# Performance work log

Measured on AMD Instinct MI355X. Metric: run time of the kernel, lower is better.

The kernel has to match this reference:

```python
import jax, jax.numpy as jnp
import numpy as np

U = 4        # num_users
B = 64       # batch
N = 2048     # n_antennas (RIS elements)
F = 4        # feature_dim per user
H = 16       # local_info_dim + global_info_dim
LD = 8       # local_info_dim
GD = 8       # global_info_dim
CIN = F + 2 * H  # 36, input channels for layers 2-7 and final conv


def setup_inputs() -> dict:
    key = jax.random.key(0)
    ks = jax.random.split(key, 12)
    w = lambda k, s: (jax.random.normal(k, s, dtype=jnp.float32) * 0.1)
    return {
        "channel": jax.random.normal(ks[0], (B, U * F, N), dtype=jnp.float32),
        "We1": w(ks[1], (H, F)), "be1": w(ks[2], (H,)),
        "We": w(ks[3], (6, H, CIN)), "be": w(ks[4], (6, H)),
        "Wo1": w(ks[5], (H, F)), "bo1": w(ks[6], (H,)),
        "Wo": w(ks[7], (6, H, CIN)), "bo": w(ks[8], (6, H)),
        "W8": w(ks[9], (1, CIN)), "b8": w(ks[10], (1,)),
        "num_users": U,
    }


def _conv1x1(f, W, b):
    # f: [U, B, Cin, N], W: [Cout, Cin] -> [U, B, Cout, N]
    return jnp.einsum('ubcn,oc->ubon', f, W) + b[None, None, :, None]


def _forward(channel, We1, be1, We, be, Wo1, bo1, Wo, bo, W8, b8, num_users):
    b_, nf, n = channel.shape
    fpu = nf // num_users
    # split per-user channel slices -> [U, B, F, N]
    ch = channel.reshape(b_, num_users, fpu, n).transpose(1, 0, 2, 3)
    feats = ch
    for i in range(7):
        We_i = We1 if i == 0 else We[i - 1]
        be_i = be1 if i == 0 else be[i - 1]
        Wo_i = Wo1 if i == 0 else Wo[i - 1]
        bo_i = bo1 if i == 0 else bo[i - 1]
        ego = jax.nn.relu(_conv1x1(feats, We_i, be_i))       # [U,B,H,N]
        opp = jax.nn.relu(_conv1x1(feats, Wo_i, bo_i))       # [U,B,H,N]
        # leave-one-out mean over users: sum-then-subtract (O(U) not O(U^2))
        loo = (jnp.sum(opp, axis=0, keepdims=True) - opp) / (num_users - 1)

        def split(o):
            g = jnp.mean(o[:, :, -GD:, :], axis=3, keepdims=True)
            g = jnp.broadcast_to(g, (num_users, b_, GD, n))
            return o[:, :, :LD, :], g

        el, eg = split(ego)
        ol, og = split(loo)
        feats = jnp.concatenate([ch, el, eg, ol, og], axis=2)  # [U,B,36,N]
    fm = jnp.mean(feats, axis=0)                              # [B,36,N]
    out = (jnp.einsum('bcn,oc->bon', fm, W8) + b8[None, :, None]) * jnp.float32(np.pi)
    return out  # [B,1,N]


def reference(channel, We1, be1, We, be, Wo1, bo1, Wo, bo, W8, b8, num_users):
    return _forward(channel, We1, be1, We, be, Wo1, bo1, Wo, bo, W8, b8, num_users)
```

## Files before the change

kernel.cpp:

```cpp
#include <hip/hip_runtime.h>
#include <hip/hip_cooperative_groups.h>

namespace cg = cooperative_groups;

#define TPB 1024
#define GRID 256


typedef float f2 __attribute__((ext_vector_type(2)));
static __device__ __forceinline__ f2 spl(float s) { f2 r; r.x = s; r.y = s; return r; }

__global__ void risnet_kernel(
    const float* __restrict__ channel,
    const float* __restrict__ We1, const float* __restrict__ be1,
    const float* __restrict__ We,  const float* __restrict__ be,
    const float* __restrict__ Wo1, const float* __restrict__ bo1,
    const float* __restrict__ Wo,  const float* __restrict__ bo,
    const float* __restrict__ W8,  const float* __restrict__ b8,
    float* __restrict__ out, float* __restrict__ part, int* __restrict__ flags)
{
  const int tid   = threadIdx.x;
  const int lane  = tid & 63;
  const int wv    = tid >> 6;
  const int p     = tid & 1;
  const int B     = blockIdx.x;
  const int b     = (B & 7) * 8 + ((B >> 3) & 7);
  const int chunk = B >> 6;
  const int n     = (chunk << 9) | (tid >> 1);

  __shared__ __align__(16) float biasE[2][16][4];
  __shared__ __align__(16) float biasO[2][16][4];
  __shared__ float red[64][64];
  __shared__ float gv[64];
  __shared__ float fin;

  if (tid == 0)
    __hip_atomic_store(&flags[B], 0, __ATOMIC_RELAXED, __HIP_MEMORY_SCOPE_AGENT);

  f2 ch2[4];
#pragma unroll
  for (int f = 0; f < 4; ++f) {
    ch2[f].x = channel[((b*4 + 2*p + 0)*4 + f)*2048 + n];
    ch2[f].y = channel[((b*4 + 2*p + 1)*4 + f)*2048 + n];
  }

  cg::grid_group grid = cg::this_grid();
  grid.sync();

  f2 el2[8], ol2[8];

#define BFLY3(a0, a1) { \
  a0 += __shfl_xor(a0, 2, 64);  a1 += __shfl_xor(a1, 2, 64);  \
  a0 += __shfl_xor(a0, 4, 64);  a1 += __shfl_xor(a1, 4, 64);  \
  a0 += __shfl_xor(a0, 8, 64);  a1 += __shfl_xor(a1, 8, 64); }

#define RED_W(base_col, a0, a1) \
  if ((lane & 15) < 2) { \
    red[(wv<<2)|(lane>>4)][(base_col) + 2*(lane&1) + 0] = a0; \
    red[(wv<<2)|(lane>>4)][(base_col) + 2*(lane&1) + 1] = a1; }

#define PUBLISH(Lpar, Lval) { \
  __syncthreads(); \
  if (tid < 64) { \
    float s0 = 0.f, s1 = 0.f, s2 = 0.f, s3 = 0.f; \
    _Pragma("unroll") for (int r = 0; r < 64; r += 4) { \
      s0 += red[r+0][tid]; s1 += red[r+1][tid]; \
      s2 += red[r+2][tid]; s3 += red[r+3][tid]; \
    } \
    __hip_atomic_store(&part[(((Lpar)*64 + b)*4 + chunk)*64 + tid], \
                       (s0+s1)+(s2+s3), \
                       __ATOMIC_RELAXED, __HIP_MEMORY_SCOPE_AGENT); \
  } \
  if (tid == 0) \
    __hip_atomic_store(&flags[B], (Lval), __ATOMIC_RELEASE, __HIP_MEMORY_SCOPE_AGENT); }

#define SPIN_RELAXED(tgt) { \
  const int gi = (B & 63) | ((lane & 3) << 6); \
  for (;;) { \
    int f = __hip_atomic_load(&flags[gi], __ATOMIC_RELAXED, __HIP_MEMORY_SCOPE_AGENT); \
    if (__all(f >= (tgt))) break; \
    __builtin_amdgcn_s_sleep(1); \
  } \
  __builtin_amdgcn_fence(__ATOMIC_ACQUIRE, "agent"); }

#define DOT20B(ACC, W0, W1, W2, W5, W6, BINIT) { \
  f2 v = (BINIT); \
  v = spl(W0.x)*ch2[0] + v; v = spl(W0.y)*ch2[1] + v; \
  v = spl(W0.z)*ch2[2] + v; v = spl(W0.w)*ch2[3] + v; \
  v = spl(W1.x)*el2[0] + v; v = spl(W1.y)*el2[1] + v; \
  v = spl(W1.z)*el2[2] + v; v = spl(W1.w)*el2[3] + v; \
  v = spl(W2.x)*el2[4] + v; v = spl(W2.y)*el2[5] + v; \
  v = spl(W2.z)*el2[6] + v; v = spl(W2.w)*el2[7] + v; \
  v = spl(W5.x)*ol2[0] + v; v = spl(W5.y)*ol2[1] + v; \
  v = spl(W5.z)*ol2[2] + v; v = spl(W5.w)*ol2[3] + v; \
  v = spl(W6.x)*ol2[4] + v; v = spl(W6.y)*ol2[5] + v; \
  v = spl(W6.z)*ol2[6] + v; v = spl(W6.w)*ol2[7] + v; \
  ACC = v; }

  {
    f2 opl2[8];
#pragma unroll
    for (int h = 0; h < 16; ++h) {
      const float4 w = *(const float4*)(We1 + h*4);
      f2 a = spl(be1[h]);
      a = spl(w.x)*ch2[0] + a; a = spl(w.y)*ch2[1] + a;
      a = spl(w.z)*ch2[2] + a; a = spl(w.w)*ch2[3] + a;
      a.x = fmaxf(a.x, 0.f); a.y = fmaxf(a.y, 0.f);
      if (h < 8) el2[h] = a;
      else { float a0 = a.x, a1 = a.y; BFLY3(a0, a1); RED_W((h-8)*4, a0, a1); }
    }
#pragma unroll
    for (int h = 0; h < 16; ++h) {
      const float4 w = *(const float4*)(Wo1 + h*4);
      f2 a = spl(bo1[h]);
      a = spl(w.x)*ch2[0] + a; a = spl(w.y)*ch2[1] + a;
      a = spl(w.z)*ch2[2] + a; a = spl(w.w)*ch2[3] + a;
      a.x = fmaxf(a.x, 0.f); a.y = fmaxf(a.y, 0.f);
      if (h < 8) opl2[h] = a;
      else { float a0 = a.x, a1 = a.y; BFLY3(a0, a1); RED_W(32 + (h-8)*4, a0, a1); }
    }
#pragma unroll
    for (int j = 0; j < 8; ++j) {
      const float s2 = opl2[j].x + opl2[j].y;
      const float s4 = s2 + __shfl_xor(s2, 1, 64);
      ol2[j] = (spl(s4) - opl2[j]) * spl(1.f/3.f);
    }
  }
  PUBLISH(0, 1)

  for (int L = 1; L < 7; ++L) {
    const float* __restrict__ wEl = We + (L-1)*576;
    const float* __restrict__ wOl = Wo + (L-1)*576;
    const int par_r = (L-1) & 1;
    const int par_w = L & 1;
    const int bb    = L & 1;

    f2 accE2[16];
#pragma unroll
    for (int h = 0; h < 16; ++h) {
      const float4* wr = (const float4*)(wEl + h*36);
      const float4 w0 = wr[0], w1 = wr[1], w2 = wr[2], w5 = wr[5], w6 = wr[6];
      DOT20B(accE2[h], w0, w1, w2, w5, w6, spl(0.f))
    }

    if (wv == 15) {
      SPIN_RELAXED(L)
      float s = 0.f;
#pragma unroll
      for (int k = 0; k < 4; ++k)
        s += __hip_atomic_load(&part[((par_r*64 + b)*4 + k)*64 + lane],
                               __ATOMIC_RELAXED, __HIP_MEMORY_SCOPE_AGENT);
      gv[lane] = s * (1.f/2048.f);
      const int u = lane & 3;
      const int h = lane >> 2;
      float bE = be[(L-1)*16 + h];
      float bO = bo[(L-1)*16 + h];
#pragma unroll
      for (int j = 0; j < 8; ++j) {
        const float eg = gv[j*4 + u];
        const float so = gv[32+j*4+0] + gv[32+j*4+1] + gv[32+j*4+2] + gv[32+j*4+3];
        const float og = (so - gv[32 + j*4 + u]) * (1.f/3.f);
        bE += wEl[h*36 + 12 + j] * eg + wEl[h*36 + 28 + j] * og;
        bO += wOl[h*36 + 12 + j] * eg + wOl[h*36 + 28 + j] * og;
      }
      biasE[bb][h][u] = bE;
      biasO[bb][h][u] = bO;
    }
    __syncthreads();

#pragma unroll
    for (int h = 8; h < 16; ++h) {
      f2 a = accE2[h] + *(const f2*)&biasE[bb][h][2*p];
      float a0 = fmaxf(a.x, 0.f), a1 = fmaxf(a.y, 0.f);
      BFLY3(a0, a1); RED_W((h-8)*4, a0, a1);
    }
#pragma unroll
    for (int h = 8; h < 16; ++h) {
      const float4* wr = (const float4*)(wOl + h*36);
      const float4 w0 = wr[0], w1 = wr[1], w2 = wr[2], w5 = wr[5], w6 = wr[6];
      f2 a;
      DOT20B(a, w0, w1, w2, w5, w6, *(const f2*)&biasO[bb][h][2*p])
      float a0 = fmaxf(a.x, 0.f), a1 = fmaxf(a.y, 0.f);
      BFLY3(a0, a1); RED_W(32 + (h-8)*4, a0, a1);
    }
    PUBLISH(par_w, L + 1)

    f2 eln2[8];
#pragma unroll
    for (int h = 0; h < 8; ++h) {
      f2 a = accE2[h] + *(const f2*)&biasE[bb][h][2*p];
      a.x = fmaxf(a.x, 0.f); a.y = fmaxf(a.y, 0.f);
      eln2[h] = a;
    }
    f2 opl2[8];
#pragma unroll
    for (int h = 0; h < 8; ++h) {
      const float4* wr = (const float4*)(wOl + h*36);
      const float4 w0 = wr[0], w1 = wr[1], w2 = wr[2], w5 = wr[5], w6 = wr[6];
      f2 a;
      DOT20B(a, w0, w1, w2, w5, w6, *(const f2*)&biasO[bb][h][2*p])
      a.x = fmaxf(a.x, 0.f); a.y = fmaxf(a.y, 0.f);
      opl2[h] = a;
    }
#pragma unroll
    for (int j = 0; j < 8; ++j) {
      const float s2 = opl2[j].x + opl2[j].y;
      const float s4 = s2 + __shfl_xor(s2, 1, 64);
      ol2[j] = (spl(s4) - opl2[j]) * spl(1.f/3.f);
      el2[j] = eln2[j];
    }
  }

  if (wv == 0) {
    SPIN_RELAXED(7)
    float s = 0.f;
#pragma unroll
    for (int k = 0; k < 4; ++k)
      s += __hip_atomic_load(&part[((0*64 + b)*4 + k)*64 + lane],
                             __ATOMIC_RELAXED, __HIP_MEMORY_SCOPE_AGENT);
    gv[lane] = s * (1.f/2048.f);
    if (lane == 0) {
      float sf = b8[0];
#pragma unroll
      for (int j = 0; j < 8; ++j) {
        const float so = gv[32+j*4+0] + gv[32+j*4+1] + gv[32+j*4+2] + gv[32+j*4+3];
#pragma unroll
        for (int u = 0; u < 4; ++u) {
          const float eg = gv[j*4 + u];
          const float og = (so - gv[32 + j*4 + u]) * (1.f/3.f);
          sf += 0.25f * (W8[12 + j] * eg + W8[28 + j] * og);
        }
      }
      fin = sf;
    }
  }
  __syncthreads();
  f2 v = spl(0.f);
#pragma unroll
  for (int c = 0; c < 4; ++c) v = spl(W8[c]) * ch2[c] + v;
#pragma unroll
  for (int j = 0; j < 8; ++j) {
    v = spl(W8[4 + j]) * el2[j] + v;
    v = spl(W8[20 + j]) * ol2[j] + v;
  }
  float t = v.x + v.y;
  t += __shfl_xor(t, 1, 64);
  if (p == 0)
    out[b*2048 + n] = (fin + 0.25f * t) * 3.14159265358979f;
}

extern "C" void kernel_launch(void* const* d_in, const int* in_sizes, int n_in,
                              void* d_out, int out_size, void* d_ws, size_t ws_size,
                              hipStream_t stream) {
  const float* channel = (const float*)d_in[0];
  const float* We1 = (const float*)d_in[1];
  const float* be1 = (const float*)d_in[2];
  const float* We  = (const float*)d_in[3];
  const float* be  = (const float*)d_in[4];
  const float* Wo1 = (const float*)d_in[5];
  const float* bo1 = (const float*)d_in[6];
  const float* Wo  = (const float*)d_in[7];
  const float* bo  = (const float*)d_in[8];
  const float* W8  = (const float*)d_in[9];
  const float* b8  = (const float*)d_in[10];
  float* out  = (float*)d_out;
  float* part = (float*)d_ws;
  int*   flags = (int*)((char*)d_ws + 131072);

  void* args[] = { (void*)&channel, (void*)&We1, (void*)&be1, (void*)&We, (void*)&be,
                   (void*)&Wo1, (void*)&bo1, (void*)&Wo, (void*)&bo,
                   (void*)&W8, (void*)&b8, (void*)&out, (void*)&part, (void*)&flags };
  hipLaunchCooperativeKernel((void*)risnet_kernel, dim3(GRID), dim3(TPB), args, 0, stream);
}
```

Baseline: 141.6 us.

## Replace block-level reduction and flag publishing with per-wave atomics and counters

Each wave now finishes its reduction across all 64 lanes with shuffles and adds its partial sums straight into a per-layer global buffer with float atomics. It then bumps a per-layer, per-batch counter, and consumers spin until that counter reaches 64 wave arrivals. This drops the shared-memory reduction array, the __syncthreads before each publish and the four-way chunk summation on the reader side. In exchange there are many more global atomic adds per layer, float sums whose order is nondeterministic, and zero-initialisation of all seven layer buffers before the grid sync.

New measurement: 406.6 us. +187.2%, slower.

```diff
diff --git a/kernel.cpp b/kernel.cpp
--- a/kernel.cpp
+++ b/kernel.cpp
@@ -17,7 +17,7 @@
     const float* __restrict__ Wo1, const float* __restrict__ bo1,
     const float* __restrict__ Wo,  const float* __restrict__ bo,
     const float* __restrict__ W8,  const float* __restrict__ b8,
-    float* __restrict__ out, float* __restrict__ part, int* __restrict__ flags)
+    float* __restrict__ out, float* __restrict__ part, int* __restrict__ cnt)
 {
   const int tid   = threadIdx.x;
   const int lane  = tid & 63;
@@ -30,12 +30,16 @@
 
   __shared__ __align__(16) float biasE[2][16][4];
   __shared__ __align__(16) float biasO[2][16][4];
-  __shared__ float red[64][64];
   __shared__ float gv[64];
   __shared__ float fin;
 
-  if (tid == 0)
-    __hip_atomic_store(&flags[B], 0, __ATOMIC_RELAXED, __HIP_MEMORY_SCOPE_AGENT);
+  {
+    const int i = B * TPB + tid;
+    if (i < 7*64*64)
+      __hip_atomic_store(&part[i], 0.f, __ATOMIC_RELAXED, __HIP_MEMORY_SCOPE_AGENT);
+    if (i < 7*64)
+      __hip_atomic_store(&cnt[i], 0, __ATOMIC_RELAXED, __HIP_MEMORY_SCOPE_AGENT);
+  }
 
   f2 ch2[4];
 #pragma unroll
@@ -49,36 +53,26 @@
 
   f2 el2[8], ol2[8];
 
-#define BFLY3(a0, a1) { \
+#define PUB5(Lb, base_col, a0, a1) { \
   a0 += __shfl_xor(a0, 2, 64);  a1 += __shfl_xor(a1, 2, 64);  \
   a0 += __shfl_xor(a0, 4, 64);  a1 += __shfl_xor(a1, 4, 64);  \
-  a0 += __shfl_xor(a0, 8, 64);  a1 += __shfl_xor(a1, 8, 64); }
-
-#define RED_W(base_col, a0, a1) \
-  if ((lane & 15) < 2) { \
-    red[(wv<<2)|(lane>>4)][(base_col) + 2*(lane&1) + 0] = a0; \
-    red[(wv<<2)|(lane>>4)][(base_col) + 2*(lane&1) + 1] = a1; }
-
-#define PUBLISH(Lpar, Lval) { \
-  __syncthreads(); \
-  if (tid < 64) { \
-    float s0 = 0.f, s1 = 0.f, s2 = 0.f, s3 = 0.f; \
-    _Pragma("unroll") for (int r = 0; r < 64; r += 4) { \
-      s0 += red[r+0][tid]; s1 += red[r+1][tid]; \
-      s2 += red[r+2][tid]; s3 += red[r+3][tid]; \
-    } \
-    __hip_atomic_store(&part[(((Lpar)*64 + b)*4 + chunk)*64 + tid], \
-                       (s0+s1)+(s2+s3), \
-                       __ATOMIC_RELAXED, __HIP_MEMORY_SCOPE_AGENT); \
-  } \
-  if (tid == 0) \
-    __hip_atomic_store(&flags[B], (Lval), __ATOMIC_RELEASE, __HIP_MEMORY_SCOPE_AGENT); }
-
-#define SPIN_RELAXED(tgt) { \
-  const int gi = (B & 63) | ((lane & 3) << 6); \
+  a0 += __shfl_xor(a0, 8, 64);  a1 += __shfl_xor(a1, 8, 64);  \
+  a0 += __shfl_xor(a0, 16, 64); a1 += __shfl_xor(a1, 16, 64); \
+  a0 += __shfl_xor(a0, 32, 64); a1 += __shfl_xor(a1, 32, 64); \
+  if (lane < 2) { \
+    unsafeAtomicAdd(&part[(Lb) + (base_col) + 2*lane + 0], a0); \
+    unsafeAtomicAdd(&part[(Lb) + (base_col) + 2*lane + 1], a1); \
+  } }
+
+#define DONE_CNT(idx) { \
+  __builtin_amdgcn_fence(__ATOMIC_RELEASE, "agent"); \
+  if (lane == 0) \
+    __hip_atomic_fetch_add(&cnt[idx], 1, __ATOMIC_RELAXED, __HIP_MEMORY_SCOPE_AGENT); }
+
+#define SPIN_CNT(idx) { \
   for (;;) { \
-    int f = __hip_atomic_load(&flags[gi], __ATOMIC_RELAXED, __HIP_MEMORY_SCOPE_AGENT); \
-    if (__all(f >= (tgt))) break; \
+    int c = __hip_atomic_load(&cnt[idx], __ATOMIC_RELAXED, __HIP_MEMORY_SCOPE_AGENT); \
+    if (c >= 64) break; \
     __builtin_amdgcn_s_sleep(1); \
   } \
   __builtin_amdgcn_fence(__ATOMIC_ACQUIRE, "agent"); }
@@ -107,7 +101,7 @@
       a = spl(w.z)*ch2[2] + a; a = spl(w.w)*ch2[3] + a;
       a.x = fmaxf(a.x, 0.f); a.y = fmaxf(a.y, 0.f);
       if (h < 8) el2[h] = a;
-      else { float a0 = a.x, a1 = a.y; BFLY3(a0, a1); RED_W((h-8)*4, a0, a1); }
+      else { float a0 = a.x, a1 = a.y; PUB5(b*64, (h-8)*4, a0, a1) }
     }
 #pragma unroll
     for (int h = 0; h < 16; ++h) {
@@ -117,8 +111,9 @@
       a = spl(w.z)*ch2[2] + a; a = spl(w.w)*ch2[3] + a;
       a.x = fmaxf(a.x, 0.f); a.y = fmaxf(a.y, 0.f);
       if (h < 8) opl2[h] = a;
-      else { float a0 = a.x, a1 = a.y; BFLY3(a0, a1); RED_W(32 + (h-8)*4, a0, a1); }
-    }
+      else { float a0 = a.x, a1 = a.y; PUB5(b*64, 32 + (h-8)*4, a0, a1) }
+    }
+    DONE_CNT(b)
 #pragma unroll
     for (int j = 0; j < 8; ++j) {
       const float s2 = opl2[j].x + opl2[j].y;
@@ -126,14 +121,12 @@
       ol2[j] = (spl(s4) - opl2[j]) * spl(1.f/3.f);
     }
   }
-  PUBLISH(0, 1)
 
   for (int L = 1; L < 7; ++L) {
     const float* __restrict__ wEl = We + (L-1)*576;
     const float* __restrict__ wOl = Wo + (L-1)*576;
-    const int par_r = (L-1) & 1;
-    const int par_w = L & 1;
-    const int bb    = L & 1;
+    const int bb = L & 1;
+    const int Lb = (L*64 + b)*64;
 
     f2 accE2[16];
 #pragma unroll
@@ -144,12 +137,9 @@
     }
 
     if (wv == 15) {
-      SPIN_RELAXED(L)
-      float s = 0.f;
-#pragma unroll
-      for (int k = 0; k < 4; ++k)
-        s += __hip_atomic_load(&part[((par_r*64 + b)*4 + k)*64 + lane],
-                               __ATOMIC_RELAXED, __HIP_MEMORY_SCOPE_AGENT);
+      SPIN_CNT((L-1)*64 + b)
+      float s = __hip_atomic_load(&part[((L-1)*64 + b)*64 + lane],
+                                  __ATOMIC_RELAXED, __HIP_MEMORY_SCOPE_AGENT);
       gv[lane] = s * (1.f/2048.f);
       const int u = lane & 3;
       const int h = lane >> 2;
@@ -172,7 +162,7 @@
     for (int h = 8; h < 16; ++h) {
       f2 a = accE2[h] + *(const f2*)&biasE[bb][h][2*p];
       float a0 = fmaxf(a.x, 0.f), a1 = fmaxf(a.y, 0.f);
-      BFLY3(a0, a1); RED_W((h-8)*4, a0, a1);
+      PUB5(Lb, (h-8)*4, a0, a1)
     }
 #pragma unroll
     for (int h = 8; h < 16; ++h) {
@@ -181,9 +171,9 @@
       f2 a;
       DOT20B(a, w0, w1, w2, w5, w6, *(const f2*)&biasO[bb][h][2*p])
       float a0 = fmaxf(a.x, 0.f), a1 = fmaxf(a.y, 0.f);
-      BFLY3(a0, a1); RED_W(32 + (h-8)*4, a0, a1);
-    }
-    PUBLISH(par_w, L + 1)
+      PUB5(Lb, 32 + (h-8)*4, a0, a1)
+    }
+    DONE_CNT(L*64 + b)
 
     f2 eln2[8];
 #pragma unroll
@@ -212,12 +202,9 @@
   }
 
   if (wv == 0) {
-    SPIN_RELAXED(7)
-    float s = 0.f;
-#pragma unroll
-    for (int k = 0; k < 4; ++k)
-      s += __hip_atomic_load(&part[((0*64 + b)*4 + k)*64 + lane],
-                             __ATOMIC_RELAXED, __HIP_MEMORY_SCOPE_AGENT);
+    SPIN_CNT(6*64 + b)
+    float s = __hip_atomic_load(&part[(6*64 + b)*64 + lane],
+                                __ATOMIC_RELAXED, __HIP_MEMORY_SCOPE_AGENT);
     gv[lane] = s * (1.f/2048.f);
     if (lane == 0) {
       float sf = b8[0];
@@ -265,10 +252,10 @@
   const float* b8  = (const float*)d_in[10];
   float* out  = (float*)d_out;
   float* part = (float*)d_ws;
-  int*   flags = (int*)((char*)d_ws + 131072);
+  int*   cnt  = (int*)((char*)d_ws + 114688);
 
   void* args[] = { (void*)&channel, (void*)&We1, (void*)&be1, (void*)&We, (void*)&be,
                    (void*)&Wo1, (void*)&bo1, (void*)&Wo, (void*)&bo,
-                   (void*)&W8, (void*)&b8, (void*)&out, (void*)&part, (void*)&flags };
+                   (void*)&W8, (void*)&b8, (void*)&out, (void*)&part, (void*)&cnt };
   hipLaunchCooperativeKernel((void*)risnet_kernel, dim3(GRID), dim3(TPB), args, 0, stream);
 }
```
